# Kernel optimization log

Measured on AMD Instinct MI355X. Metric: run time of the kernel, lower is better.

The kernel has to match this reference:

```python
import jax, jax.numpy as jnp
import numpy as np

N, E, F, T = 10000, 160000, 4, 12   # nodes, edges, features, periods
C, HID, OUT = 512, 256, 12          # tgcn out_channels, head hidden, output_dim


def setup_inputs() -> dict:
    key = jax.random.key(0)
    ks = jax.random.split(key, 24)
    g = lambda k, s: (jax.random.normal(k, s, dtype=jnp.float32) * 0.05)
    inp = {
        "x": jax.random.normal(ks[0], (N, F, T), dtype=jnp.float32),
        "edge_index": jax.random.randint(ks[1], (2, E), 0, N, dtype=jnp.int32),
        "edge_attr": jax.random.uniform(ks[2], (E,), dtype=jnp.float32),
        "att": g(ks[3], (T,)),
        # TGCN gates: GCNConv (W [F,C], b [C]) + Linear on cat([conv, H]) ([2C,C], [C])
        "Wz_g": g(ks[4], (F, C)), "bz_g": jnp.zeros((C,), jnp.float32),
        "Wz_l": g(ks[5], (2 * C, C)), "bz_l": jnp.zeros((C,), jnp.float32),
        "Wr_g": g(ks[6], (F, C)), "br_g": jnp.zeros((C,), jnp.float32),
        "Wr_l": g(ks[7], (2 * C, C)), "br_l": jnp.zeros((C,), jnp.float32),
        "Wh_g": g(ks[8], (F, C)), "bh_g": jnp.zeros((C,), jnp.float32),
        "Wh_l": g(ks[9], (2 * C, C)), "bh_l": jnp.zeros((C,), jnp.float32),
        # dense head
        "W1": g(ks[10], (C, HID)), "b1": jnp.zeros((HID,), jnp.float32),
        "W2": g(ks[11], (HID, OUT)), "b2": jnp.zeros((OUT,), jnp.float32),
    }
    return inp


def reference(x, edge_index, edge_attr, att,
              Wz_g, bz_g, Wz_l, bz_l,
              Wr_g, br_g, Wr_l, br_l,
              Wh_g, bh_g, Wh_l, bh_l,
              W1, b1, W2, b2):
    n = x.shape[0]
    # GCN normalization with self loops (fill value 1.0), computed once
    loops = jnp.arange(n, dtype=edge_index.dtype)
    src = jnp.concatenate([edge_index[0], loops])
    dst = jnp.concatenate([edge_index[1], loops])
    w = jnp.concatenate([edge_attr, jnp.ones((n,), x.dtype)])
    deg = jax.ops.segment_sum(w, dst, num_segments=n)
    dinv = jax.lax.rsqrt(jnp.maximum(deg, 1e-12))
    norm = dinv[src] * w * dinv[dst]  # [E+N]

    def gcn(xt, W, b):
        xw = xt @ W                                   # [N,C]
        msg = norm[:, None] * xw[src]                 # gather over edges
        return jax.ops.segment_sum(msg, dst, num_segments=n) + b

    probs = jax.nn.softmax(att)            # attention over periods
    xt_seq = jnp.moveaxis(x, -1, 0)        # [T,N,F]
    H0 = jnp.zeros((n, C), x.dtype)

    def step(carry, inp):
        H, acc = carry
        xt, p = inp
        z = jax.nn.sigmoid(jnp.concatenate([gcn(xt, Wz_g, bz_g), H], axis=1) @ Wz_l + bz_l)
        r = jax.nn.sigmoid(jnp.concatenate([gcn(xt, Wr_g, br_g), H], axis=1) @ Wr_l + br_l)
        ht = jnp.tanh(jnp.concatenate([gcn(xt, Wh_g, bh_g), H * r], axis=1) @ Wh_l + bh_l)
        Hn = z * H + (1.0 - z) * ht
        return (Hn, acc + p * Hn), None

    (Hf, H_accum), _ = jax.lax.scan(step, (H0, H0), (xt_seq, probs))
    out_hidden = H_accum
    h = jax.nn.relu(H_accum)
    h = jax.nn.relu(h @ W1 + b1)
    h = h @ W2 + b2
    return (h, out_hidden)
```

## Files before the change

### kernel.cpp

```cpp
#include <hip/hip_runtime.h>
#include <math.h>

#define NF 48
#define TT 12

typedef __bf16 v8bf __attribute__((ext_vector_type(8)));
typedef float v16f __attribute__((ext_vector_type(16)));

__device__ __forceinline__ void gld16(const void* g, void* l) {
  __builtin_amdgcn_global_load_lds(
      (const __attribute__((address_space(1))) void*)(uintptr_t)g,
      (__attribute__((address_space(3))) void*)(uintptr_t)l, 16, 0, 0);
}


__global__ void k_init(float* __restrict__ deg, int* __restrict__ cnt, int n) {
  int i = blockIdx.x * blockDim.x + threadIdx.x;
  if (i < n) { deg[i] = 1.0f; cnt[i] = 0; cnt[n + i] = 0; }
}

__global__ void k_edge(const int* __restrict__ dst, const float* __restrict__ w,
                       float* __restrict__ deg, int* __restrict__ cnt, int e) {
  int i = blockIdx.x * blockDim.x + threadIdx.x;
  if (i < e) {
    int d = dst[i];
    atomicAdd(&deg[d], w[i]);
    atomicAdd(&cnt[d], 1);
  }
}


__global__ void k_scan1(const int* __restrict__ cnt, int* __restrict__ pscan,
                        int* __restrict__ bsum, const float* __restrict__ deg,
                        float* __restrict__ dinv, int n) {
  __shared__ int s[256];
  int i = blockIdx.x * 256 + threadIdx.x;
  int v = (i < n) ? cnt[i] : 0;
  s[threadIdx.x] = v;
  __syncthreads();
  for (int off = 1; off < 256; off <<= 1) {
    int t = 0;
    if (threadIdx.x >= off) t = s[threadIdx.x - off];
    __syncthreads();
    s[threadIdx.x] += t;
    __syncthreads();
  }
  if (i < n) {
    pscan[i] = s[threadIdx.x] - v;
    dinv[i] = rsqrtf(fmaxf(deg[i], 1e-12f));
  }
  if (threadIdx.x == 255) bsum[blockIdx.x] = s[255];
}

__global__ void k_scan2(const int* __restrict__ bsum, int* __restrict__ bpre, int nb,
                        const float* __restrict__ att, float* __restrict__ probs) {
  if (blockIdx.x == 0 && threadIdx.x == 0) {
    int run = 0;
    for (int b = 0; b < nb; b++) { bpre[b] = run; run += bsum[b]; }
  }
  if (blockIdx.x == 0 && threadIdx.x == 64) {
    float m = -1e30f;
    for (int t = 0; t < TT; t++) m = fmaxf(m, att[t]);
    float e[TT], s = 0.f;
    for (int t = 0; t < TT; t++) { e[t] = expf(att[t] - m); s += e[t]; }
    for (int t = 0; t < TT; t++) probs[t] = e[t] / s;
  }
}

__global__ void k_scan3(const int* __restrict__ pscan, const int* __restrict__ bpre,
                        int* __restrict__ offs, int n, int e) {
  int i = blockIdx.x * blockDim.x + threadIdx.x;
  if (i < n) offs[i] = pscan[i] + bpre[i >> 8];
  if (i == 0) offs[n] = e;
}

__global__ void k_place(const int* __restrict__ src, const int* __restrict__ dst,
                        const float* __restrict__ w, const int* __restrict__ offs,
                        int* __restrict__ fill, int* __restrict__ csrc,
                        float* __restrict__ cw, int e) {
  int i = blockIdx.x * blockDim.x + threadIdx.x;
  if (i >= e) return;
  int d = dst[i];
  int p = offs[d] + atomicAdd(&fill[d], 1);
  csrc[p] = src[i];
  cw[p] = w[i];
}

__global__ void k_gather(const int* __restrict__ offs, const int* __restrict__ csrc,
                         const float* __restrict__ cw, const float* __restrict__ dinv,
                         const float* __restrict__ x, float* __restrict__ Y, int n) {
  int tg = blockIdx.x * blockDim.x + threadIdx.x;
  if (tg >= n * 12) return;
  int i = tg / 12, q = tg % 12;
  float di = dinv[i];
  const float4* x4 = (const float4*)x;
  float4 sv = x4[(size_t)i * 12 + q];
  float ax = di * sv.x, ay = di * sv.y, az = di * sv.z, aw = di * sv.w;
  int e1 = offs[i + 1];
  for (int e = offs[i]; e < e1; e++) {
    int s = csrc[e];
    float wv = cw[e] * dinv[s];
    float4 xv = x4[(size_t)s * 12 + q];
    ax = fmaf(wv, xv.x, ax); ay = fmaf(wv, xv.y, ay);
    az = fmaf(wv, xv.z, az); aw = fmaf(wv, xv.w, aw);
  }
  float4 o = make_float4(di * ax, di * ay, di * az, di * aw);
  ((float4*)Y)[(size_t)i * 12 + q] = o;
}

__device__ __forceinline__ size_t packIdx128(int n, int k) {
  int row = n & 127;
  int c = (k & 31) >> 3;
  return (size_t)(n >> 7) * (128 * 512) + (size_t)(k >> 5) * (128 * 32) +
         (size_t)row * 32 + (size_t)((c ^ ((row >> 1) & 3)) << 3) + (k & 7);
}

__global__ void k_pack3(const float* __restrict__ Wzl, const float* __restrict__ Wrl,
                        const float* __restrict__ Whl, const float* __restrict__ W1,
                        __bf16* __restrict__ WzrP, __bf16* __restrict__ WhP,
                        __bf16* __restrict__ W1P) {
  __shared__ __bf16 t[64][72];
  int modew = blockIdx.z;
  if (modew == 1 && blockIdx.x >= 8) return;
  if (modew == 2 && blockIdx.x >= 4) return;
  int n0 = blockIdx.x * 64, k0 = blockIdx.y * 64;
  __bf16* WT = (modew == 0) ? WzrP : (modew == 1) ? WhP : W1P;
#pragma unroll
  for (int p = 0; p < 4; p++) {
    int kk = p * 16 + (threadIdx.x >> 4);
    int nn = (threadIdx.x & 15) * 4;
    int n = n0 + nn, k = k0 + kk;
    float4 v;
    if (modew == 2) {
      v = *(const float4*)(W1 + (size_t)k * 256 + n);
    } else {
      const float* src = (modew == 1) ? Whl : Wzl;
      int nc = n;
      if (modew == 0 && n >= 512) { src = Wrl; nc = n - 512; }
      v = *(const float4*)(src + (size_t)(512 + k) * 512 + nc);
    }
    t[kk][nn + 0] = (__bf16)v.x; t[kk][nn + 1] = (__bf16)v.y;
    t[kk][nn + 2] = (__bf16)v.z; t[kk][nn + 3] = (__bf16)v.w;
  }
  __syncthreads();
#pragma unroll
  for (int u = 0; u < 2; u++) {
    int unit = threadIdx.x * 2 + u;
    int nl = unit >> 3, kg = unit & 7;
    v8bf o;
#pragma unroll
    for (int j = 0; j < 8; j++) o[j] = t[kg * 8 + j][nl];
    *(v8bf*)(WT + packIdx128(n0 + nl, k0 + kg * 8)) = o;
  }
}

__global__ void k_build_eff3(const float* __restrict__ Wzg, const float* __restrict__ Wzl,
                             const float* __restrict__ bzg, const float* __restrict__ bzl,
                             const float* __restrict__ Wrg, const float* __restrict__ Wrl,
                             const float* __restrict__ brg, const float* __restrict__ brl,
                             const float* __restrict__ Whg, const float* __restrict__ Whl,
                             const float* __restrict__ bhg, const float* __restrict__ bhl,
                             float* __restrict__ WzrE, float* __restrict__ bzrE,
                             float* __restrict__ WhE, float* __restrict__ bhE) {
  int idx = blockIdx.x * blockDim.x + threadIdx.x;
  if (idx >= 3 * 5 * 512) return;
  int seg = idx / 2560;
  int r = (idx % 2560) / 512, c = idx % 512;
  const float *Wg, *Wl, *bg, *bl;
  float *We, *be;
  int ostride, ooff;
  if (seg == 0) { Wg = Wzg; Wl = Wzl; bg = bzg; bl = bzl; We = WzrE; be = bzrE; ostride = 1024; ooff = 0; }
  else if (seg == 1) { Wg = Wrg; Wl = Wrl; bg = brg; bl = brl; We = WzrE; be = bzrE; ostride = 1024; ooff = 512; }
  else { Wg = Whg; Wl = Whl; bg = bhg; bl = bhl; We = WhE; be = bhE; ostride = 512; ooff = 0; }
  float s = 0.f;
  if (r < 4) {
    for (int k = 0; k < 512; k++) s += Wg[r * 512 + k] * Wl[k * 512 + c];
    We[r * ostride + ooff + c] = s;
  } else {
    for (int k = 0; k < 512; k++) s += bg[k] * Wl[k * 512 + c];
    be[ooff + c] = s + bl[c];
  }
}

__global__ void k_wy3(const float* __restrict__ WzrE, const float* __restrict__ bzrE,
                      const float* __restrict__ WhE, const float* __restrict__ bhE,
                      const float* __restrict__ b1,
                      __bf16* __restrict__ WyZR, __bf16* __restrict__ WyH,
                      __bf16* __restrict__ Wy1) {
  int idx = blockIdx.x * blockDim.x + threadIdx.x;
  const float* Weff; const float* beff; __bf16* out; int Nout, loc;
  if (idx < 1024 * 16) { Weff = WzrE; beff = bzrE; out = WyZR; Nout = 1024; loc = idx; }
  else if (idx < (1024 + 512) * 16) { Weff = WhE; beff = bhE; out = WyH; Nout = 512; loc = idx - 1024 * 16; }
  else if (idx < (1024 + 512 + 256) * 16) { Weff = nullptr; beff = b1; out = Wy1; Nout = 256; loc = idx - (1024 + 512) * 16; }
  else return;
  int n = loc >> 4, k = loc & 15;
  float v = 0.f;
  if (k < 4) v = Weff ? Weff[k * Nout + n] : 0.f;
  else if (k == 4) v = beff[n];
  out[(size_t)(n >> 7) * 2048 + (size_t)(n & 127) * 16 + k] = (__bf16)v;
}

__global__ void k_yat0(const float* __restrict__ Y,
                       const float* __restrict__ WzrE, const float* __restrict__ bzrE,
                       const float* __restrict__ WhE, const float* __restrict__ bhE,
                       __bf16* __restrict__ Ya, __bf16* __restrict__ H1, int n) {
  int idx = blockIdx.x * blockDim.x + threadIdx.x;
  int nt0 = n * 512;
  if (idx < nt0) {
    int i = idx >> 9, c = idx & 511;
    float y0 = Y[(size_t)i * NF + 0], y1 = Y[(size_t)i * NF + 12];
    float y2 = Y[(size_t)i * NF + 24], y3 = Y[(size_t)i * NF + 36];
    float pz = bzrE[c] + y0 * WzrE[c] + y1 * WzrE[1024 + c] +
               y2 * WzrE[2048 + c] + y3 * WzrE[3072 + c];
    float ph = bhE[c] + y0 * WhE[c] + y1 * WhE[512 + c] +
               y2 * WhE[1024 + c] + y3 * WhE[1536 + c];
    float z = 1.f / (1.f + expf(-pz));
    H1[idx] = (__bf16)((1.f - z) * tanhf(ph));
  } else {
    int r = idx - nt0;
    if (r >= TT * n * 16) return;
    int t = r / (n * 16);
    int loc = r % (n * 16);
    int nn = loc >> 4, k = loc & 15;
    float v = 0.f;
    if (k < 4) v = Y[(size_t)nn * NF + k * TT + t];
    else if (k == 4) v = 1.f;
    Ya[r] = (__bf16)v;
  }
}

template <int MODE>
__global__ __launch_bounds__(256, 4) void k_mm(
    const __bf16* __restrict__ Agm, const __bf16* __restrict__ Bp,
    const __bf16* __restrict__ Hc, const __bf16* __restrict__ Zbf,
    const __bf16* __restrict__ Ay, const __bf16* __restrict__ Wy,
    float* __restrict__ Ofp, __bf16* __restrict__ Obf, __bf16* __restrict__ ObfR,
    int M, int RB) {
  constexpr int BUFS = 6144;
  __shared__ __bf16 smem[18432];

  const int RBX = (RB + 7) >> 3;
  int xcd = blockIdx.x & 7;
  int idx = blockIdx.x >> 3;
  int rowblk = xcd * RBX + idx % RBX;
  int colblk = idx / RBX;
  if (rowblk >= RB) return;

  const int row0 = rowblk * 64;
  const int tid = threadIdx.x;
  const int lane = tid & 63, w = tid >> 6;
  const int wr = (w >> 1) * 32, wc = (w & 1) * 64;
  const int l31 = lane & 31, lh = lane >> 5;

  const int ar = tid >> 2, ac = tid & 3;
  const __bf16* At = Agm + (size_t)(row0 + ar) * 512 + ((ac ^ ((ar >> 1) & 3)) << 3);
  const __bf16* Bt = Bp + (size_t)colblk * (128 * 512);

  v16f acc[2];
#pragma unroll
  for (int j = 0; j < 2; j++)
#pragma unroll
    for (int q = 0; q < 16; q++) acc[j][q] = 0.f;

  auto stage = [&](int buf, int kt) {
    __bf16* base = smem + buf * BUFS;
    gld16(At + kt * 32, base + w * 512);
    const __bf16* bs = Bt + (size_t)kt * 4096 + (size_t)tid * 8;
    gld16(bs, base + 2048 + w * 512);
    gld16(bs + 2048, base + 4096 + w * 512);
  };
  auto compute = [&](int buf) {
    const __bf16* base = smem + buf * BUFS;
    __builtin_amdgcn_s_setprio(1);
#pragma unroll
    for (int ks = 0; ks < 2; ks++) {
      int kc = ks * 2 + lh;
      int fr = wr + l31;
      v8bf a = *(const v8bf*)&base[fr * 32 + ((kc ^ ((fr >> 1) & 3)) << 3)];
#pragma unroll
      for (int ni = 0; ni < 2; ni++) {
        int fc = wc + ni * 32 + l31;
        v8bf b = *(const v8bf*)&base[2048 + fc * 32 + ((kc ^ ((fc >> 1) & 3)) << 3)];
        acc[ni] = __builtin_amdgcn_mfma_f32_32x32x16_bf16(a, b, acc[ni], 0, 0, 0);
      }
    }
    __builtin_amdgcn_s_setprio(0);
  };

  v8bf ya = *(const v8bf*)(Ay + (size_t)(row0 + wr + l31) * 16 + lh * 8);
  v8bf yb0 = *(const v8bf*)(Wy + (size_t)colblk * 2048 + (size_t)(wc + l31) * 16 + lh * 8);
  v8bf yb1 = *(const v8bf*)(Wy + (size_t)colblk * 2048 + (size_t)(wc + 32 + l31) * 16 + lh * 8);
  stage(0, 0);
  stage(1, 1);
#pragma unroll
  for (int kt = 0; kt < 16; kt++) {
    if (kt < 15)
      asm volatile("s_waitcnt vmcnt(3) lgkmcnt(0)\n\ts_barrier" ::: "memory");
    else
      asm volatile("s_waitcnt vmcnt(0) lgkmcnt(0)\n\ts_barrier" ::: "memory");
    if (kt < 14) stage((kt + 2) % 3, kt + 2);
    compute(kt % 3);
  }
  acc[0] = __builtin_amdgcn_mfma_f32_32x32x16_bf16(ya, yb0, acc[0], 0, 0, 0);
  acc[1] = __builtin_amdgcn_mfma_f32_32x32x16_bf16(ya, yb1, acc[1], 0, 0, 0);
  __syncthreads();

  if constexpr (MODE == 2) {
#pragma unroll
    for (int ni = 0; ni < 2; ni++) {
      int cl = wc + ni * 32 + l31;
#pragma unroll
      for (int reg = 0; reg < 16; reg++) {
        int rg = row0 + wr + (reg & 3) + ((reg >> 2) << 3) + (lh << 2);
        if (rg >= M) continue;
        Ofp[(size_t)rg * 256 + colblk * 128 + cl] = fmaxf(acc[ni][reg], 0.f);
      }
    }
  } else if constexpr (MODE == 0) {
#pragma unroll
    for (int ni = 0; ni < 2; ni++) {
      int cl = wc + ni * 32 + l31;
#pragma unroll
      for (int reg = 0; reg < 16; reg++) {
        int lr = wr + (reg & 3) + ((reg >> 2) << 3) + (lh << 2);
        smem[lr * 128 + cl] = (__bf16)(1.f / (1.f + expf(-acc[ni][reg])));
      }
    }
    __syncthreads();
    int row = tid >> 2, seg = (tid & 3) * 32;
    int rg = row0 + row;
    if (rg < M) {
      int cof = (colblk & 3) * 128;
      if (colblk < 4) {
#pragma unroll
        for (int q = 0; q < 4; q++) {
          uint4 v = *(const uint4*)&smem[row * 128 + seg + q * 8];
          *(uint4*)(Obf + (size_t)rg * 512 + cof + seg + q * 8) = v;
        }
      } else {
#pragma unroll
        for (int q = 0; q < 4; q++) {
          v8bf r8 = *(const v8bf*)&smem[row * 128 + seg + q * 8];
          v8bf h8 = *(const v8bf*)(Agm + (size_t)rg * 512 + cof + seg + q * 8);
          v8bf o;
#pragma unroll
          for (int j = 0; j < 8; j++) o[j] = (__bf16)((float)r8[j] * (float)h8[j]);
          *(v8bf*)(ObfR + (size_t)rg * 512 + cof + seg + q * 8) = o;
        }
      }
    }
  } else {
    float* sF = (float*)smem;
#pragma unroll
    for (int h = 0; h < 2; h++) {
      if ((w >> 1) == h) {
#pragma unroll
        for (int ni = 0; ni < 2; ni++) {
          int cl = wc + ni * 32 + l31;
#pragma unroll
          for (int reg = 0; reg < 16; reg++) {
            int lr = (reg & 3) + ((reg >> 2) << 3) + (lh << 2);
            sF[lr * 128 + cl] = tanhf(acc[ni][reg]);
          }
        }
      }
      __syncthreads();
      int row = tid >> 3, seg = (tid & 7) * 16;
      int rg = row0 + h * 32 + row;
      if (rg < M) {
        int cg0 = colblk * 128 + seg;
#pragma unroll
        for (int q = 0; q < 2; q++) {
          v8bf z8 = *(const v8bf*)(Zbf + (size_t)rg * 512 + cg0 + q * 8);
          v8bf h8 = *(const v8bf*)(Hc + (size_t)rg * 512 + cg0 + q * 8);
          v8bf o;
#pragma unroll
          for (int j = 0; j < 8; j++) {
            float z = (float)z8[j];
            float ht = sF[row * 128 + seg + q * 8 + j];
            o[j] = (__bf16)(z * (float)h8[j] + (1.f - z) * ht);
          }
          *(v8bf*)(Obf + (size_t)rg * 512 + cg0 + q * 8) = o;
        }
      }
      if (h == 0) __syncthreads();
    }
  }
}

__global__ void k_acc(const __bf16* __restrict__ hist, const float* __restrict__ probs,
                      float* __restrict__ acc, __bf16* __restrict__ accRelu, int n) {
  int idx = blockIdx.x * blockDim.x + threadIdx.x;
  if (idx >= n * 64) return;
  size_t off = (size_t)idx * 8;
  size_t S = (size_t)n * 512;
  float s[8] = {0, 0, 0, 0, 0, 0, 0, 0};
#pragma unroll
  for (int t = 0; t < TT; t++) {
    float p = probs[t];
    v8bf h = *(const v8bf*)(hist + (size_t)(t + 1) * S + off);
#pragma unroll
    for (int j = 0; j < 8; j++) s[j] = fmaf(p, (float)h[j], s[j]);
  }
  *(float4*)(acc + off) = make_float4(s[0], s[1], s[2], s[3]);
  *(float4*)(acc + off + 4) = make_float4(s[4], s[5], s[6], s[7]);
  v8bf rl;
#pragma unroll
  for (int j = 0; j < 8; j++) rl[j] = (__bf16)fmaxf(s[j], 0.f);
  *(v8bf*)(accRelu + off) = rl;
}

__global__ void k_head2(const float* __restrict__ T1, const float* __restrict__ W2,
                        const float* __restrict__ b2, float* __restrict__ out0, int M) {
  int idx = blockIdx.x * blockDim.x + threadIdx.x;
  if (idx >= M * 12) return;
  int i = idx / 12, c = idx % 12;
  const float* tr = T1 + (size_t)i * 256;
  float s = b2[c];
  for (int k = 0; k < 256; k++) s = fmaf(tr[k], W2[k * 12 + c], s);
  out0[idx] = s;
}


extern "C" void kernel_launch(void* const* d_in, const int* in_sizes, int n_in,
                              void* d_out, int out_size, void* d_ws, size_t ws_size,
                              hipStream_t stream) {
  const float* x   = (const float*)d_in[0];
  const int*   ei  = (const int*)d_in[1];
  const float* ea  = (const float*)d_in[2];
  const float* att = (const float*)d_in[3];
  const float* Wzg = (const float*)d_in[4];  const float* bzg = (const float*)d_in[5];
  const float* Wzl = (const float*)d_in[6];  const float* bzl = (const float*)d_in[7];
  const float* Wrg = (const float*)d_in[8];  const float* brg = (const float*)d_in[9];
  const float* Wrl = (const float*)d_in[10]; const float* brl = (const float*)d_in[11];
  const float* Whg = (const float*)d_in[12]; const float* bhg = (const float*)d_in[13];
  const float* Whl = (const float*)d_in[14]; const float* bhl = (const float*)d_in[15];
  const float* W1  = (const float*)d_in[16]; const float* b1  = (const float*)d_in[17];
  const float* W2  = (const float*)d_in[18]; const float* b2  = (const float*)d_in[19];

  const int N = in_sizes[0] / NF;
  const int E = in_sizes[1] / 2;
  const int* srcI = ei;
  const int* dstI = ei + E;

  float* out0 = (float*)d_out;
  float* accO = (float*)d_out + (size_t)N * 12;

  char* wp = (char*)d_ws;
  auto carve = [&](size_t bytes) -> void* {
    void* p = (void*)wp;
    wp += (bytes + 255) & ~(size_t)255;
    return p;
  };
  float*  deg     = (float*)carve((size_t)N * 4);
  float*  dinv    = (float*)carve((size_t)N * 4);
  float*  probs   = (float*)carve(64);
  float*  Y       = (float*)carve((size_t)N * NF * 4);
  __bf16* WzrP    = (__bf16*)carve((size_t)1024 * 512 * 2);
  __bf16* WhP     = (__bf16*)carve((size_t)512 * 512 * 2);
  __bf16* W1P     = (__bf16*)carve((size_t)256 * 512 * 2);
  float*  Wzr_eff = (float*)carve((size_t)4 * 1024 * 4);
  float*  bzr_eff = (float*)carve((size_t)1024 * 4);
  float*  Wh_eff  = (float*)carve((size_t)4 * 512 * 4);
  float*  bh_eff  = (float*)carve((size_t)512 * 4);
  __bf16* hist    = (__bf16*)carve((size_t)(TT + 1) * N * 512 * 2);
  __bf16* Zbf     = (__bf16*)carve((size_t)N * 512 * 2);
  __bf16* Rbf     = (__bf16*)carve((size_t)N * 512 * 2);
  __bf16* accRelu = (__bf16*)carve((size_t)N * 512 * 2);
  float*  T1      = (float*)carve((size_t)N * 256 * 4);
  __bf16* Ya      = (__bf16*)carve((size_t)TT * N * 16 * 2);
  __bf16* WyZR    = (__bf16*)carve((size_t)1024 * 16 * 2);
  __bf16* WyH     = (__bf16*)carve((size_t)512 * 16 * 2);
  __bf16* Wy1     = (__bf16*)carve((size_t)256 * 16 * 2);
  int*    cnt     = (int*)carve((size_t)2 * N * 4);
  int*    fill    = cnt + N;
  int*    offs    = (int*)carve((size_t)(N + 1) * 4);
  int*    pscan   = (int*)carve((size_t)N * 4);
  int*    bsum    = (int*)carve(256);
  int*    bpre    = (int*)carve(256);
  int*    csrc    = (int*)carve((size_t)E * 4);
  float*  cw      = (float*)carve((size_t)E * 4);
  (void)carve(512 * 1024);
  (void)ws_size; (void)n_in; (void)out_size;

  const int TPB = 256;
  auto cdiv = [](int a, int b) { return (a + b - 1) / b; };
  const size_t S = (size_t)N * 512;

  k_init<<<cdiv(N, TPB), TPB, 0, stream>>>(deg, cnt, N);
  k_edge<<<cdiv(E, TPB), TPB, 0, stream>>>(dstI, ea, deg, cnt, E);

  const int nb = cdiv(N, 256);
  k_scan1<<<nb, 256, 0, stream>>>(cnt, pscan, bsum, deg, dinv, N);
  k_scan2<<<1, 128, 0, stream>>>(bsum, bpre, nb, att, probs);
  k_scan3<<<cdiv(N, TPB), TPB, 0, stream>>>(pscan, bpre, offs, N, E);
  k_place<<<cdiv(E, TPB), TPB, 0, stream>>>(srcI, dstI, ea, offs, fill, csrc, cw, E);
  k_gather<<<cdiv(N * 12, TPB), TPB, 0, stream>>>(offs, csrc, cw, dinv, x, Y, N);

  {
    dim3 gp(16, 8, 3);
    k_pack3<<<gp, 256, 0, stream>>>(Wzl, Wrl, Whl, W1, WzrP, WhP, W1P);
  }
  k_build_eff3<<<cdiv(3 * 5 * 512, TPB), TPB, 0, stream>>>(
      Wzg, Wzl, bzg, bzl, Wrg, Wrl, brg, brl, Whg, Whl, bhg, bhl,
      Wzr_eff, bzr_eff, Wh_eff, bh_eff);
  k_wy3<<<cdiv((1024 + 512 + 256) * 16, TPB), TPB, 0, stream>>>(
      Wzr_eff, bzr_eff, Wh_eff, bh_eff, b1, WyZR, WyH, Wy1);

  k_yat0<<<cdiv(N * 512 + TT * N * 16, TPB), TPB, 0, stream>>>(
      Y, Wzr_eff, bzr_eff, Wh_eff, bh_eff, Ya, hist + S, N);

  const int RB = cdiv(N, 64);
  const int RBX = cdiv(RB, 8);
  for (int t = 1; t < TT; t++) {
    const __bf16* Hbt = hist + (size_t)t * S;
    __bf16* Hbn = hist + (size_t)(t + 1) * S;
    const __bf16* Yat = Ya + (size_t)t * N * 16;
    k_mm<0><<<8 * RBX * 8, 256, 0, stream>>>(Hbt, WzrP, nullptr, nullptr, Yat, WyZR,
                                             nullptr, Zbf, Rbf, N, RB);
    k_mm<1><<<8 * RBX * 4, 256, 0, stream>>>(Rbf, WhP, Hbt, Zbf, Yat, WyH,
                                             nullptr, Hbn, nullptr, N, RB);
  }

  k_acc<<<cdiv(N * 64, TPB), TPB, 0, stream>>>(hist, probs, accO, accRelu, N);
  k_mm<2><<<8 * RBX * 2, 256, 0, stream>>>(accRelu, W1P, nullptr, nullptr, Ya, Wy1,
                                           T1, nullptr, nullptr, N, RB);
  k_head2<<<cdiv(N * 12, TPB), TPB, 0, stream>>>(T1, W2, b2, out0, N);
}
```

Measured before the change: 671.8 us.

## Double GEMM row tile to 128 so each B fragment feeds two A fragments

Each k_mm block now covers 128 rows instead of 64, and every wave computes a 64x64 output tile as 2x2 MFMA accumulators. Each loaded B fragment is reused across two A fragments, and each block's B tile is amortized over more rows. Shared memory per block grows, launch bounds drop from 4 to 3 blocks per CU, and the grid halves. With about 79 row blocks, fewer blocks may leave CUs idle and reduce latency hiding. Loads past row N in the staged A tiles and Ay rely on padded buffers, as the previous tiling already did.

```diff
diff --git a/kernel.cpp b/kernel.cpp
--- a/kernel.cpp
+++ b/kernel.cpp
@@ -230,14 +230,14 @@
 }
 
 template <int MODE>
-__global__ __launch_bounds__(256, 4) void k_mm(
+__global__ __launch_bounds__(256, 3) void k_mm(
     const __bf16* __restrict__ Agm, const __bf16* __restrict__ Bp,
     const __bf16* __restrict__ Hc, const __bf16* __restrict__ Zbf,
     const __bf16* __restrict__ Ay, const __bf16* __restrict__ Wy,
     float* __restrict__ Ofp, __bf16* __restrict__ Obf, __bf16* __restrict__ ObfR,
     int M, int RB) {
-  constexpr int BUFS = 6144;
-  __shared__ __bf16 smem[18432];
+  constexpr int BUFS = 8192;
+  __shared__ __bf16 smem[24576];
 
   const int RBX = (RB + 7) >> 3;
   int xcd = blockIdx.x & 7;
@@ -246,28 +246,32 @@
   int colblk = idx / RBX;
   if (rowblk >= RB) return;
 
-  const int row0 = rowblk * 64;
+  const int row0 = rowblk * 128;
   const int tid = threadIdx.x;
   const int lane = tid & 63, w = tid >> 6;
-  const int wr = (w >> 1) * 32, wc = (w & 1) * 64;
+  const int wr = (w >> 1) * 64, wc = (w & 1) * 64;
   const int l31 = lane & 31, lh = lane >> 5;
 
   const int ar = tid >> 2, ac = tid & 3;
-  const __bf16* At = Agm + (size_t)(row0 + ar) * 512 + ((ac ^ ((ar >> 1) & 3)) << 3);
+  const __bf16* At0 = Agm + (size_t)(row0 + ar) * 512 + ((ac ^ ((ar >> 1) & 3)) << 3);
+  const __bf16* At1 = Agm + (size_t)(row0 + 64 + ar) * 512 + ((ac ^ ((ar >> 1) & 3)) << 3);
   const __bf16* Bt = Bp + (size_t)colblk * (128 * 512);
 
-  v16f acc[2];
-#pragma unroll
-  for (int j = 0; j < 2; j++)
-#pragma unroll
-    for (int q = 0; q < 16; q++) acc[j][q] = 0.f;
+  v16f acc[2][2];
+#pragma unroll
+  for (int ri = 0; ri < 2; ri++)
+#pragma unroll
+    for (int ni = 0; ni < 2; ni++)
+#pragma unroll
+      for (int q = 0; q < 16; q++) acc[ri][ni][q] = 0.f;
 
   auto stage = [&](int buf, int kt) {
     __bf16* base = smem + buf * BUFS;
-    gld16(At + kt * 32, base + w * 512);
+    gld16(At0 + kt * 32, base + w * 512);
+    gld16(At1 + kt * 32, base + 2048 + w * 512);
     const __bf16* bs = Bt + (size_t)kt * 4096 + (size_t)tid * 8;
-    gld16(bs, base + 2048 + w * 512);
-    gld16(bs + 2048, base + 4096 + w * 512);
+    gld16(bs, base + 4096 + w * 512);
+    gld16(bs + 2048, base + 6144 + w * 512);
   };
   auto compute = [&](int buf) {
     const __bf16* base = smem + buf * BUFS;
@@ -275,19 +279,22 @@
 #pragma unroll
     for (int ks = 0; ks < 2; ks++) {
       int kc = ks * 2 + lh;
-      int fr = wr + l31;
-      v8bf a = *(const v8bf*)&base[fr * 32 + ((kc ^ ((fr >> 1) & 3)) << 3)];
+      int fr0 = wr + l31, fr1 = wr + 32 + l31;
+      v8bf a0 = *(const v8bf*)&base[fr0 * 32 + ((kc ^ ((fr0 >> 1) & 3)) << 3)];
+      v8bf a1 = *(const v8bf*)&base[fr1 * 32 + ((kc ^ ((fr1 >> 1) & 3)) << 3)];
 #pragma unroll
       for (int ni = 0; ni < 2; ni++) {
         int fc = wc + ni * 32 + l31;
-        v8bf b = *(const v8bf*)&base[2048 + fc * 32 + ((kc ^ ((fc >> 1) & 3)) << 3)];
-        acc[ni] = __builtin_amdgcn_mfma_f32_32x32x16_bf16(a, b, acc[ni], 0, 0, 0);
+        v8bf b = *(const v8bf*)&base[4096 + fc * 32 + ((kc ^ ((fc >> 1) & 3)) << 3)];
+        acc[0][ni] = __builtin_amdgcn_mfma_f32_32x32x16_bf16(a0, b, acc[0][ni], 0, 0, 0);
+        acc[1][ni] = __builtin_amdgcn_mfma_f32_32x32x16_bf16(a1, b, acc[1][ni], 0, 0, 0);
       }
     }
     __builtin_amdgcn_s_setprio(0);
   };
 
-  v8bf ya = *(const v8bf*)(Ay + (size_t)(row0 + wr + l31) * 16 + lh * 8);
+  v8bf ya0 = *(const v8bf*)(Ay + (size_t)(row0 + wr + l31) * 16 + lh * 8);
+  v8bf ya1 = *(const v8bf*)(Ay + (size_t)(row0 + wr + 32 + l31) * 16 + lh * 8);
   v8bf yb0 = *(const v8bf*)(Wy + (size_t)colblk * 2048 + (size_t)(wc + l31) * 16 + lh * 8);
   v8bf yb1 = *(const v8bf*)(Wy + (size_t)colblk * 2048 + (size_t)(wc + 32 + l31) * 16 + lh * 8);
   stage(0, 0);
@@ -295,51 +302,57 @@
 #pragma unroll
   for (int kt = 0; kt < 16; kt++) {
     if (kt < 15)
-      asm volatile("s_waitcnt vmcnt(3) lgkmcnt(0)\n\ts_barrier" ::: "memory");
+      asm volatile("s_waitcnt vmcnt(4) lgkmcnt(0)\n\ts_barrier" ::: "memory");
     else
       asm volatile("s_waitcnt vmcnt(0) lgkmcnt(0)\n\ts_barrier" ::: "memory");
     if (kt < 14) stage((kt + 2) % 3, kt + 2);
     compute(kt % 3);
   }
-  acc[0] = __builtin_amdgcn_mfma_f32_32x32x16_bf16(ya, yb0, acc[0], 0, 0, 0);
-  acc[1] = __builtin_amdgcn_mfma_f32_32x32x16_bf16(ya, yb1, acc[1], 0, 0, 0);
+  acc[0][0] = __builtin_amdgcn_mfma_f32_32x32x16_bf16(ya0, yb0, acc[0][0], 0, 0, 0);
+  acc[0][1] = __builtin_amdgcn_mfma_f32_32x32x16_bf16(ya0, yb1, acc[0][1], 0, 0, 0);
+  acc[1][0] = __builtin_amdgcn_mfma_f32_32x32x16_bf16(ya1, yb0, acc[1][0], 0, 0, 0);
+  acc[1][1] = __builtin_amdgcn_mfma_f32_32x32x16_bf16(ya1, yb1, acc[1][1], 0, 0, 0);
   __syncthreads();
 
   if constexpr (MODE == 2) {
 #pragma unroll
-    for (int ni = 0; ni < 2; ni++) {
-      int cl = wc + ni * 32 + l31;
-#pragma unroll
-      for (int reg = 0; reg < 16; reg++) {
-        int rg = row0 + wr + (reg & 3) + ((reg >> 2) << 3) + (lh << 2);
-        if (rg >= M) continue;
-        Ofp[(size_t)rg * 256 + colblk * 128 + cl] = fmaxf(acc[ni][reg], 0.f);
+    for (int ri = 0; ri < 2; ri++)
+#pragma unroll
+      for (int ni = 0; ni < 2; ni++) {
+        int cl = colblk * 128 + wc + ni * 32 + l31;
+#pragma unroll
+        for (int reg = 0; reg < 16; reg++) {
+          int rg = row0 + wr + ri * 32 + (reg & 3) + ((reg >> 2) << 3) + (lh << 2);
+          if (rg >= M) continue;
+          Ofp[(size_t)rg * 256 + cl] = fmaxf(acc[ri][ni][reg], 0.f);
+        }
       }
-    }
   } else if constexpr (MODE == 0) {
 #pragma unroll
-    for (int ni = 0; ni < 2; ni++) {
-      int cl = wc + ni * 32 + l31;
-#pragma unroll
-      for (int reg = 0; reg < 16; reg++) {
-        int lr = wr + (reg & 3) + ((reg >> 2) << 3) + (lh << 2);
-        smem[lr * 128 + cl] = (__bf16)(1.f / (1.f + expf(-acc[ni][reg])));
+    for (int ri = 0; ri < 2; ri++)
+#pragma unroll
+      for (int ni = 0; ni < 2; ni++) {
+        int cl = wc + ni * 32 + l31;
+#pragma unroll
+        for (int reg = 0; reg < 16; reg++) {
+          int lr = wr + ri * 32 + (reg & 3) + ((reg >> 2) << 3) + (lh << 2);
+          smem[lr * 128 + cl] = (__bf16)(1.f / (1.f + expf(-acc[ri][ni][reg])));
+        }
       }
-    }
     __syncthreads();
-    int row = tid >> 2, seg = (tid & 3) * 32;
+    int row = tid >> 1, seg = (tid & 1) * 64;
     int rg = row0 + row;
     if (rg < M) {
       int cof = (colblk & 3) * 128;
       if (colblk < 4) {
 #pragma unroll
-        for (int q = 0; q < 4; q++) {
+        for (int q = 0; q < 8; q++) {
           uint4 v = *(const uint4*)&smem[row * 128 + seg + q * 8];
           *(uint4*)(Obf + (size_t)rg * 512 + cof + seg + q * 8) = v;
         }
       } else {
 #pragma unroll
-        for (int q = 0; q < 4; q++) {
+        for (int q = 0; q < 8; q++) {
           v8bf r8 = *(const v8bf*)&smem[row * 128 + seg + q * 8];
           v8bf h8 = *(const v8bf*)(Agm + (size_t)rg * 512 + cof + seg + q * 8);
           v8bf o;
@@ -352,25 +365,27 @@
   } else {
     float* sF = (float*)smem;
 #pragma unroll
-    for (int h = 0; h < 2; h++) {
-      if ((w >> 1) == h) {
-#pragma unroll
-        for (int ni = 0; ni < 2; ni++) {
-          int cl = wc + ni * 32 + l31;
-#pragma unroll
-          for (int reg = 0; reg < 16; reg++) {
-            int lr = (reg & 3) + ((reg >> 2) << 3) + (lh << 2);
-            sF[lr * 128 + cl] = tanhf(acc[ni][reg]);
+    for (int p = 0; p < 2; p++) {
+      if ((w >> 1) == p) {
+#pragma unroll
+        for (int ri = 0; ri < 2; ri++)
+#pragma unroll
+          for (int ni = 0; ni < 2; ni++) {
+            int cl = wc + ni * 32 + l31;
+#pragma unroll
+            for (int reg = 0; reg < 16; reg++) {
+              int lr = ri * 32 + (reg & 3) + ((reg >> 2) << 3) + (lh << 2);
+              sF[lr * 128 + cl] = tanhf(acc[ri][ni][reg]);
+            }
           }
-        }
       }
       __syncthreads();
-      int row = tid >> 3, seg = (tid & 7) * 16;
-      int rg = row0 + h * 32 + row;
+      int row = tid >> 2, seg = (tid & 3) * 32;
+      int rg = row0 + p * 64 + row;
       if (rg < M) {
         int cg0 = colblk * 128 + seg;
 #pragma unroll
-        for (int q = 0; q < 2; q++) {
+        for (int q = 0; q < 4; q++) {
           v8bf z8 = *(const v8bf*)(Zbf + (size_t)rg * 512 + cg0 + q * 8);
           v8bf h8 = *(const v8bf*)(Hc + (size_t)rg * 512 + cg0 + q * 8);
           v8bf o;
@@ -383,7 +398,7 @@
           *(v8bf*)(Obf + (size_t)rg * 512 + cg0 + q * 8) = o;
         }
       }
-      if (h == 0) __syncthreads();
+      if (p == 0) __syncthreads();
     }
   }
 }
@@ -510,7 +525,7 @@
   k_yat0<<<cdiv(N * 512 + TT * N * 16, TPB), TPB, 0, stream>>>(
       Y, Wzr_eff, bzr_eff, Wh_eff, bh_eff, Ya, hist + S, N);
 
-  const int RB = cdiv(N, 64);
+  const int RB = cdiv(N, 128);
   const int RBX = cdiv(RB, 8);
   for (int t = 1; t < TT; t++) {
     const __bf16* Hbt = hist + (size_t)t * S;
```

New measurement: 794.1 us. 1.18x slower.
